# Kernel tuning notes

Hardware: AMD Instinct MI355X
Metric: run time of the kernel (lower is better)

## Reference

```python
import jax, jax.numpy as jnp
import numpy as np

DIM = 1024          # dim_feature
NUM_CLUSTERS = 8
N_PER = 4096        # patches per cluster (equal-size clusters)
NUM_SAMPLE = 1024   # num_sample_feature
QDIM = 128          # q projection dim
# sample_ratio = NUM_SAMPLE / (NUM_CLUSTERS*N_PER) = 1/32 -> top_k per cluster
TOPK = int(np.rint(N_PER * NUM_SAMPLE / (NUM_CLUSTERS * N_PER)))  # 128


def setup_inputs() -> dict:
    key = jax.random.key(0)
    ks = jax.random.split(key, 6)
    s = 1.0 / np.sqrt(DIM)
    return {
        "cluster_features": jax.random.normal(ks[0], (NUM_CLUSTERS, N_PER, DIM), jnp.float32),
        "key_feats": jax.random.normal(ks[1], (NUM_CLUSTERS, 1, DIM), jnp.float32),
        "q_w": jax.random.normal(ks[2], (QDIM, DIM), jnp.float32) * s,
        "q_b": jax.random.normal(ks[3], (QDIM,), jnp.float32) * 0.01,
        "v_w": jax.random.normal(ks[4], (DIM, DIM), jnp.float32) * s,
        "v_b": jax.random.normal(ks[5], (DIM,), jnp.float32) * 0.01,
    }


def reference(cluster_features, key_feats, q_w, q_b, v_w, v_b):
    scale_q = jnp.sqrt(jnp.float32(QDIM))

    def per_cluster(feats, key_feat):
        # NonLocalRanking with top_k=TOPK, top_fuse=False (adaptive path)
        Q = feats @ q_w.T + q_b            # [N, 128]
        qk = key_feat @ q_w.T + q_b        # [1, 128]
        A = (Q @ qk.T) / scale_q           # [N, 1]
        A = jax.nn.softmax(A, axis=0)      # softmax over patches (dim 0)
        _, idx = jax.lax.top_k(A[:, 0], TOPK)
        top_feats = feats[idx]             # [TOPK, DIM]
        V = feats @ v_w.T + v_b            # [N, DIM]
        fusion = (A.T @ V)[0]              # [DIM]
        return top_feats, fusion

    tops, fus = jax.vmap(per_cluster)(cluster_features, key_feats)
    selected = tops.reshape(-1, DIM)       # [NUM_CLUSTERS*TOPK, DIM] == [NUM_SAMPLE, DIM]
    # module pads/truncates to NUM_SAMPLE; here it is exactly NUM_SAMPLE
    selected = selected[:NUM_SAMPLE]
    return selected, fus
```

## Files before the change

### kernel.cpp

```cpp
#include <hip/hip_runtime.h>
#include <math.h>


#define DIM   1024
#define NC    8
#define NPER  4096
#define QD    128
#define TOPK  128
#define K1B   128

typedef unsigned long long u64;
typedef __attribute__((ext_vector_type(2))) unsigned long long ull2;
typedef __attribute__((ext_vector_type(4))) float f4;

__global__ __launch_bounds__(256) void k0_prep(
    const float* __restrict__ key_feats, const float* __restrict__ q_w,
    const float* __restrict__ q_b, float* __restrict__ w_all)
{
    const int c  = blockIdx.x >> 2, jc = blockIdx.x & 3;
    const int tid = threadIdx.x;
    __shared__ float part[256];
    __shared__ float qs[QD];

    {
        const int k = tid >> 1, half = tid & 1;
        const float4* qr4 = (const float4*)(q_w + (size_t)k * DIM + half * 512);
        const float4* kf4 = (const float4*)(key_feats + (size_t)c * DIM + half * 512);
        float s = 0.f;
        #pragma unroll 16
        for (int j = 0; j < 128; ++j) {
            float4 a = qr4[j], b = kf4[j];
            s += a.x*b.x + a.y*b.y + a.z*b.z + a.w*b.w;
        }
        part[tid] = s;
    }
    __syncthreads();
    if (tid < QD) qs[tid] = part[2*tid] + part[2*tid+1] + q_b[tid];
    __syncthreads();

    const int j = jc * 256 + tid;
    float s = 0.f;
    #pragma unroll 16
    for (int k = 0; k < QD; ++k)
        s += q_w[(size_t)k * DIM + j] * qs[k];
    w_all[c * DIM + j] = s * 0.08838834764831845f;
}

__global__ __launch_bounds__(256, 4) void k1_main(
    const float* __restrict__ feats, const float* __restrict__ w_all,
    u64* __restrict__ keys,
    float* __restrict__ pacc,
    float* __restrict__ pm, float* __restrict__ pz)
{
    const int c    = blockIdx.y;
    const int blk  = blockIdx.x;
    const int tid  = threadIdx.x;
    const int lane = tid & 63;
    const int wave = tid >> 6;

    const float4* w4 = (const float4*)(w_all + c * DIM);
    float4 wv[4];
    #pragma unroll
    for (int q = 0; q < 4; ++q) wv[q] = w4[lane + 64*q];

    float4 acc[4];
    #pragma unroll
    for (int q = 0; q < 4; ++q) acc[q] = make_float4(0.f, 0.f, 0.f, 0.f);
    float m = -INFINITY, Z = 0.f;

    const int wslot = blk * 4 + wave;
    const float* fc = feats + (size_t)c * NPER * DIM;

    f4 fA[4], fB[4];
    {
        const f4* f4p = (const f4*)(fc + (size_t)wslot * DIM);
        #pragma unroll
        for (int q = 0; q < 4; ++q) fA[q] = __builtin_nontemporal_load(f4p + lane + 64*q);
    }

    #define K1_PROCESS(FREG, ROW)                                              \
    do {                                                                       \
        float p = 0.f;                                                         \
        _Pragma("unroll")                                                      \
        for (int q = 0; q < 4; ++q)                                            \
            p += FREG[q].x*wv[q].x + FREG[q].y*wv[q].y +                       \
                 FREG[q].z*wv[q].z + FREG[q].w*wv[q].w;                        \
        _Pragma("unroll")                                                      \
        for (int off = 32; off > 0; off >>= 1) p += __shfl_xor(p, off, 64);    \
        if (lane == 0) {                                                       \
            unsigned int b = __float_as_uint(p);                               \
            unsigned int u = b ^ ((b & 0x80000000u) ? 0xFFFFFFFFu : 0x80000000u); \
            keys[c * NPER + (ROW)] = ((u64)u << 32) | (unsigned int)(~(ROW));  \
        }                                                                      \
        if (p > m) {                  \
            const float sOld = __expf(m - p);                                  \
            Z = Z * sOld + 1.f;                                                \
            _Pragma("unroll")                                                  \
            for (int q = 0; q < 4; ++q) {                                      \
                acc[q].x = acc[q].x * sOld + FREG[q].x;                        \
                acc[q].y = acc[q].y * sOld + FREG[q].y;                        \
                acc[q].z = acc[q].z * sOld + FREG[q].z;                        \
                acc[q].w = acc[q].w * sOld + FREG[q].w;                        \
            }                                                                  \
            m = p;                                                             \
        } else {                                                               \
            const float t = __expf(p - m);                                     \
            Z += t;                                                            \
            _Pragma("unroll")                                                  \
            for (int q = 0; q < 4; ++q) {                                      \
                acc[q].x += t * FREG[q].x;                                     \
                acc[q].y += t * FREG[q].y;                                     \
                acc[q].z += t * FREG[q].z;                                     \
                acc[q].w += t * FREG[q].w;                                     \
            }                                                                  \
        }                                                                      \
    } while (0)

    for (int it = 0; it < 8; it += 2) {
        const int r0 = wslot + 512 * it;
        {
            const f4* f4p = (const f4*)(fc + (size_t)(r0 + 512) * DIM);
            #pragma unroll
            for (int q = 0; q < 4; ++q) fB[q] = __builtin_nontemporal_load(f4p + lane + 64*q);
        }
        K1_PROCESS(fA, r0);
        if (it + 2 < 8) {
            const f4* f4p = (const f4*)(fc + (size_t)(r0 + 1024) * DIM);
            #pragma unroll
            for (int q = 0; q < 4; ++q) fA[q] = __builtin_nontemporal_load(f4p + lane + 64*q);
        }
        K1_PROCESS(fB, r0 + 512);
    }
    #undef K1_PROCESS

    __shared__ float sm[4], sz[4];
    __shared__ float sacc[4][DIM];
    if (lane == 0) { sm[wave] = m; sz[wave] = Z; }
    #pragma unroll
    for (int q = 0; q < 4; ++q)
        ((float4*)sacc[wave])[lane + 64*q] = acc[q];
    __syncthreads();

    const float mb = fmaxf(fmaxf(sm[0], sm[1]), fmaxf(sm[2], sm[3]));
    const float e0 = __expf(sm[0] - mb), e1 = __expf(sm[1] - mb);
    const float e2 = __expf(sm[2] - mb), e3 = __expf(sm[3] - mb);
    float4 a0 = ((float4*)sacc[0])[tid];
    float4 a1 = ((float4*)sacc[1])[tid];
    float4 a2 = ((float4*)sacc[2])[tid];
    float4 a3 = ((float4*)sacc[3])[tid];
    float4 o;
    o.x = a0.x*e0 + a1.x*e1 + a2.x*e2 + a3.x*e3;
    o.y = a0.y*e0 + a1.y*e1 + a2.y*e2 + a3.y*e3;
    o.z = a0.z*e0 + a1.z*e1 + a2.z*e2 + a3.z*e3;
    o.w = a0.w*e0 + a1.w*e1 + a2.w*e2 + a3.w*e3;
    ((float4*)(pacc + (size_t)(c * K1B + blk) * DIM))[tid] = o;
    if (tid == 0) {
        pm[c * K1B + blk] = mb;
        pz[c * K1B + blk] = sz[0]*e0 + sz[1]*e1 + sz[2]*e2 + sz[3]*e3;
    }
}

__global__ __launch_bounds__(256) void fat_a(
    const float* __restrict__ pacc, const float* __restrict__ pm,
    const float* __restrict__ pz, float* __restrict__ g,
    const u64* __restrict__ keys, int* __restrict__ selIdx)
{
    const int tid = threadIdx.x;
    if (blockIdx.x < 32) {
        const int c = blockIdx.x >> 2, jb = blockIdx.x & 3;
        const int slot = tid & 63;
        const int bg   = tid >> 6;
        __shared__ float spm[K1B], spz[K1B], swe[K1B];
        __shared__ float szc;
        __shared__ float4 sred[3][64];

        if (tid < K1B) spm[tid] = pm[c*K1B + tid];
        else spz[tid - K1B] = pz[c*K1B + tid - K1B];
        __syncthreads();
        float mc = -INFINITY;
        for (int b = 0; b < K1B; ++b) mc = fmaxf(mc, spm[b]);
        if (tid < K1B) swe[tid] = __expf(spm[tid] - mc);
        __syncthreads();
        if (tid == 0) {
            float z = 0.f;
            for (int b = 0; b < K1B; ++b) z += spz[b] * swe[b];
            szc = z;
        }

        const int jbase = jb * 256 + slot * 4;
        float4 a = make_float4(0.f, 0.f, 0.f, 0.f);
        #pragma unroll
        for (int k = 0; k < 32; ++k) {
            const int b = bg * 32 + k;
            const float e = swe[b];
            float4 v = *(const float4*)(pacc + (size_t)(c*K1B + b) * DIM + jbase);
            a.x += e*v.x; a.y += e*v.y; a.z += e*v.z; a.w += e*v.w;
        }
        if (bg) sred[bg-1][slot] = a;
        __syncthreads();
        if (bg == 0) {
            float4 t0 = sred[0][slot], t1 = sred[1][slot], t2 = sred[2][slot];
            const float inv = 1.0f / szc;
            float4 o;
            o.x = (a.x + t0.x + t1.x + t2.x) * inv;
            o.y = (a.y + t0.y + t1.y + t2.y) * inv;
            o.z = (a.z + t0.z + t1.z + t2.z) * inv;
            o.w = (a.w + t0.w + t1.w + t2.w) * inv;
            *(float4*)(g + c * DIM + jbase) = o;
        }
    } else {
        const int c = blockIdx.x - 32;
        __shared__ u64 lk[NPER];
        __shared__ int hist[4096];
        __shared__ unsigned short cand[NPER];
        __shared__ int chunkSuf[256];
        __shared__ int critBin, candCnt;

        for (int t = tid; t < NPER/2; t += 256)
            ((ull2*)lk)[t] = ((const ull2*)(keys + (size_t)c * NPER))[t];
        for (int t = tid; t < 4096; t += 256) hist[t] = 0;
        if (tid == 0) candCnt = 0;
        __syncthreads();

        #pragma unroll
        for (int q = 0; q < 16; ++q)
            atomicAdd(&hist[(int)(lk[tid + 256*q] >> 52)], 1);
        __syncthreads();

        {
            int s = 0;
            #pragma unroll
            for (int b = 0; b < 16; ++b) s += hist[tid*16 + b];
            chunkSuf[tid] = s;
        }
        __syncthreads();
        if (tid == 0) {
            int run = 0;
            for (int t = 255; t >= 0; --t) {
                const int v = chunkSuf[t]; chunkSuf[t] = run; run += v;
            }
        }
        __syncthreads();
        {
            int run = chunkSuf[tid];
            for (int b = 15; b >= 0; --b) {
                const int bin = tid*16 + b;
                const int h = hist[bin];
                if (run < TOPK && run + h >= TOPK) critBin = bin;
                run += h;
            }
        }
        __syncthreads();
        const int B = critBin;

        #pragma unroll
        for (int q = 0; q < 16; ++q) {
            const int i = tid + 256*q;
            if ((int)(lk[i] >> 52) >= B) {
                const int s = atomicAdd(&candCnt, 1);
                cand[s] = (unsigned short)i;
            }
        }
        __syncthreads();

        const int M = candCnt;
        for (int s = tid; s < M; s += 256) {
            const int i = (int)cand[s];
            const u64 ki = lk[i];
            int r = 0;
            for (int j = 0; j < M; ++j)
                r += (lk[(int)cand[j]] > ki) ? 1 : 0;
            if (r < TOPK) selIdx[c * TOPK + r] = i;
        }
    }
}

__global__ __launch_bounds__(256) void fat_b(
    const int* __restrict__ selIdx, const float* __restrict__ feats,
    float* __restrict__ out_sel,
    const float* __restrict__ v_w, const float* __restrict__ v_b,
    const float* __restrict__ g, float* __restrict__ fus)
{
    const int tid = threadIdx.x;
    if (blockIdx.x < 128) {
        const int c  = blockIdx.x >> 4;
        const int r0 = (blockIdx.x & 15) * 8;
        const float* fc = feats + (size_t)c * NPER * DIM;
        const int* sic = selIdx + c * TOPK + r0;

        f4 cur = __builtin_nontemporal_load(
            (const f4*)(fc + (size_t)sic[0] * DIM) + tid);
        #pragma unroll
        for (int s = 0; s < 8; ++s) {
            f4 nxt;
            if (s + 1 < 8)
                nxt = __builtin_nontemporal_load(
                    (const f4*)(fc + (size_t)sic[s+1] * DIM) + tid);
            __builtin_nontemporal_store(
                cur, (f4*)(out_sel + ((size_t)c * TOPK + r0 + s) * DIM) + tid);
            if (s + 1 < 8) cur = nxt;
        }
    } else {
        __shared__ float4 sg[NC][256];
        const int lane = tid & 63, wave = tid >> 6;
        for (int t = tid; t < NC * 256; t += 256)
            ((float4*)sg)[t] = ((const float4*)g)[t];
        __syncthreads();

        const int row0 = (blockIdx.x - 128) * 8 + wave * 2;
        for (int rr = 0; rr < 2; ++rr) {
            const int o = row0 + rr;
            const float4* vr = (const float4*)(v_w + (size_t)o * DIM);
            float4 v[4];
            #pragma unroll
            for (int u = 0; u < 4; ++u) v[u] = vr[lane + 64*u];
            float p[NC];
            #pragma unroll
            for (int cc = 0; cc < NC; ++cc) {
                float s = 0.f;
                #pragma unroll
                for (int u = 0; u < 4; ++u) {
                    float4 gv = sg[cc][lane + 64*u];
                    s += v[u].x*gv.x + v[u].y*gv.y + v[u].z*gv.z + v[u].w*gv.w;
                }
                p[cc] = s;
            }
            #pragma unroll
            for (int off = 32; off > 0; off >>= 1) {
                #pragma unroll
                for (int cc = 0; cc < NC; ++cc) p[cc] += __shfl_xor(p[cc], off, 64);
            }
            if (lane == 0) {
                const float b = v_b[o];
                #pragma unroll
                for (int cc = 0; cc < NC; ++cc) fus[cc * DIM + o] = p[cc] + b;
            }
        }
    }
}

extern "C" void kernel_launch(void* const* d_in, const int* in_sizes, int n_in,
                              void* d_out, int out_size, void* d_ws, size_t ws_size,
                              hipStream_t stream) {
    const float* feats     = (const float*)d_in[0];
    const float* key_feats = (const float*)d_in[1];
    const float* q_w       = (const float*)d_in[2];
    const float* q_b       = (const float*)d_in[3];
    const float* v_w       = (const float*)d_in[4];
    const float* v_b       = (const float*)d_in[5];
    float* out      = (float*)d_out;
    float* out_sel  = out;
    float* out_fus  = out + (size_t)1024 * 1024;

    u64*   keys   = (u64*)d_ws;
    float* pacc   = (float*)(keys + NC * NPER);
    float* pm     = pacc + (size_t)NC * K1B * DIM;
    float* pz     = pm + NC * K1B;
    float* g      = pz + NC * K1B;
    float* w_all  = g + NC * DIM;
    int*   selIdx = (int*)(w_all + NC * DIM);

    k0_prep <<<dim3(NC * 4),  256, 0, stream>>>(key_feats, q_w, q_b, w_all);
    k1_main <<<dim3(K1B, NC), 256, 0, stream>>>(feats, w_all, keys, pacc, pm, pz);
    fat_a   <<<dim3(32 + NC), 256, 0, stream>>>(pacc, pm, pz, g, keys, selIdx);
    fat_b   <<<dim3(256),     256, 0, stream>>>(selIdx, feats, out_sel, v_w, v_b, g, out_fus);
}
```

Baseline: 235.7 us.

## Fuse reduce/top-k and gather/projection kernels via cooperative grid sync

Merges the two tail kernels into one cooperative kernel with a grid-wide barrier, removing a launch boundary. The fusion reduction is spread across 128 blocks instead of 32, and blocks that are idle in phase one prefetch their v_w rows into registers before the barrier. The cost is cooperative launch overhead, a grid sync, and a larger shared-memory union that may limit co-residency.

```diff
diff --git a/kernel.cpp b/kernel.cpp
--- a/kernel.cpp
+++ b/kernel.cpp
@@ -1,5 +1,8 @@
 #include <hip/hip_runtime.h>
+#include <hip/hip_cooperative_groups.h>
 #include <math.h>
+
+namespace cg = cooperative_groups;
 
 
 #define DIM   1024
@@ -160,22 +163,39 @@
     }
 }
 
-__global__ __launch_bounds__(256) void fat_a(
+__global__ __launch_bounds__(256) void fat_ab(
     const float* __restrict__ pacc, const float* __restrict__ pm,
     const float* __restrict__ pz, float* __restrict__ g,
-    const u64* __restrict__ keys, int* __restrict__ selIdx)
+    const u64* __restrict__ keys, int* __restrict__ selIdx,
+    const float* __restrict__ feats, float* __restrict__ out_sel,
+    const float* __restrict__ v_w, const float* __restrict__ v_b,
+    float* __restrict__ fus)
 {
+    const int bid = blockIdx.x;
     const int tid = threadIdx.x;
-    if (blockIdx.x < 32) {
-        const int c = blockIdx.x >> 2, jb = blockIdx.x & 3;
-        const int slot = tid & 63;
-        const int bg   = tid >> 6;
-        __shared__ float spm[K1B], spz[K1B], swe[K1B];
-        __shared__ float szc;
-        __shared__ float4 sred[3][64];
-
-        if (tid < K1B) spm[tid] = pm[c*K1B + tid];
-        else spz[tid - K1B] = pz[c*K1B + tid - K1B];
+    __shared__ float4 shraw4[3649];
+
+    float4 vpre0[4], vpre1[4];
+    const bool kpre = (bid >= 136);
+    if (kpre) {
+        const int lane = tid & 63, wave = tid >> 6;
+        const int row0 = (bid - 128) * 8 + wave * 2;
+        const float4* vr0 = (const float4*)(v_w + (size_t)row0 * DIM);
+        const float4* vr1 = (const float4*)(v_w + (size_t)(row0 + 1) * DIM);
+        #pragma unroll
+        for (int u = 0; u < 4; ++u) { vpre0[u] = vr0[lane + 64*u]; vpre1[u] = vr1[lane + 64*u]; }
+    }
+
+    if (bid < 128) {
+        const int c = bid >> 4, jb = bid & 15;
+        float* spm = (float*)shraw4;
+        float* spz = spm + 128;
+        float* swe = spz + 128;
+        float* szc = swe + 128;
+        float4* sred = (float4*)(szc + 4);
+
+        if (tid < K1B)       spm[tid]       = pm[c*K1B + tid];
+        else                 spz[tid - K1B] = pz[c*K1B + tid - K1B];
         __syncthreads();
         float mc = -INFINITY;
         for (int b = 0; b < K1B; ++b) mc = fmaxf(mc, spm[b]);
@@ -184,42 +204,45 @@
         if (tid == 0) {
             float z = 0.f;
             for (int b = 0; b < K1B; ++b) z += spz[b] * swe[b];
-            szc = z;
-        }
-
-        const int jbase = jb * 256 + slot * 4;
+            *szc = z;
+        }
+        const int col = tid & 15;
+        const int bg  = tid >> 4;
+        const int jbase = jb * 64 + col * 4;
         float4 a = make_float4(0.f, 0.f, 0.f, 0.f);
         #pragma unroll
-        for (int k = 0; k < 32; ++k) {
-            const int b = bg * 32 + k;
+        for (int k = 0; k < 8; ++k) {
+            const int b = bg * 8 + k;
             const float e = swe[b];
             float4 v = *(const float4*)(pacc + (size_t)(c*K1B + b) * DIM + jbase);
             a.x += e*v.x; a.y += e*v.y; a.z += e*v.z; a.w += e*v.w;
         }
-        if (bg) sred[bg-1][slot] = a;
-        __syncthreads();
-        if (bg == 0) {
-            float4 t0 = sred[0][slot], t1 = sred[1][slot], t2 = sred[2][slot];
-            const float inv = 1.0f / szc;
-            float4 o;
-            o.x = (a.x + t0.x + t1.x + t2.x) * inv;
-            o.y = (a.y + t0.y + t1.y + t2.y) * inv;
-            o.z = (a.z + t0.z + t1.z + t2.z) * inv;
-            o.w = (a.w + t0.w + t1.w + t2.w) * inv;
-            *(float4*)(g + c * DIM + jbase) = o;
-        }
-    } else {
-        const int c = blockIdx.x - 32;
-        __shared__ u64 lk[NPER];
-        __shared__ int hist[4096];
-        __shared__ unsigned short cand[NPER];
-        __shared__ int chunkSuf[256];
-        __shared__ int critBin, candCnt;
+        sred[bg * 16 + col] = a;
+        __syncthreads();
+        if (tid < 16) {
+            float4 o = make_float4(0.f, 0.f, 0.f, 0.f);
+            #pragma unroll
+            for (int gg = 0; gg < 16; ++gg) {
+                float4 t = sred[gg * 16 + tid];
+                o.x += t.x; o.y += t.y; o.z += t.z; o.w += t.w;
+            }
+            const float inv = 1.0f / (*szc);
+            o.x *= inv; o.y *= inv; o.z *= inv; o.w *= inv;
+            *(float4*)(g + c * DIM + jb * 64 + tid * 4) = o;
+        }
+    } else if (bid < 136) {
+        const int c = bid - 128;
+        u64* lk = (u64*)shraw4;
+        int* hist = (int*)(lk + NPER);
+        unsigned short* cand = (unsigned short*)(hist + 4096);
+        int* chunkSuf = (int*)(cand + NPER);
+        int* critBin = chunkSuf + 256;
+        int* candCnt = critBin + 1;
 
         for (int t = tid; t < NPER/2; t += 256)
             ((ull2*)lk)[t] = ((const ull2*)(keys + (size_t)c * NPER))[t];
         for (int t = tid; t < 4096; t += 256) hist[t] = 0;
-        if (tid == 0) candCnt = 0;
+        if (tid == 0) *candCnt = 0;
         __syncthreads();
 
         #pragma unroll
@@ -246,24 +269,24 @@
             for (int b = 15; b >= 0; --b) {
                 const int bin = tid*16 + b;
                 const int h = hist[bin];
-                if (run < TOPK && run + h >= TOPK) critBin = bin;
+                if (run < TOPK && run + h >= TOPK) *critBin = bin;
                 run += h;
             }
         }
         __syncthreads();
-        const int B = critBin;
+        const int B = *critBin;
 
         #pragma unroll
         for (int q = 0; q < 16; ++q) {
             const int i = tid + 256*q;
             if ((int)(lk[i] >> 52) >= B) {
-                const int s = atomicAdd(&candCnt, 1);
+                const int s = atomicAdd(candCnt, 1);
                 cand[s] = (unsigned short)i;
             }
         }
         __syncthreads();
 
-        const int M = candCnt;
+        const int M = *candCnt;
         for (int s = tid; s < M; s += 256) {
             const int i = (int)cand[s];
             const u64 ki = lk[i];
@@ -273,18 +296,13 @@
             if (r < TOPK) selIdx[c * TOPK + r] = i;
         }
     }
-}
-
-__global__ __launch_bounds__(256) void fat_b(
-    const int* __restrict__ selIdx, const float* __restrict__ feats,
-    float* __restrict__ out_sel,
-    const float* __restrict__ v_w, const float* __restrict__ v_b,
-    const float* __restrict__ g, float* __restrict__ fus)
-{
-    const int tid = threadIdx.x;
-    if (blockIdx.x < 128) {
-        const int c  = blockIdx.x >> 4;
-        const int r0 = (blockIdx.x & 15) * 8;
+
+    __threadfence();
+    cg::this_grid().sync();
+
+    if (bid < 128) {
+        const int c  = bid >> 4;
+        const int r0 = (bid & 15) * 8;
         const float* fc = feats + (size_t)c * NPER * DIM;
         const int* sic = selIdx + c * TOPK + r0;
 
@@ -301,26 +319,33 @@
             if (s + 1 < 8) cur = nxt;
         }
     } else {
-        __shared__ float4 sg[NC][256];
+        float4* sg = shraw4;
         const int lane = tid & 63, wave = tid >> 6;
+        __syncthreads();
         for (int t = tid; t < NC * 256; t += 256)
-            ((float4*)sg)[t] = ((const float4*)g)[t];
-        __syncthreads();
-
-        const int row0 = (blockIdx.x - 128) * 8 + wave * 2;
+            sg[t] = ((const float4*)g)[t];
+        __syncthreads();
+
+        const int row0 = (bid - 128) * 8 + wave * 2;
+        #pragma unroll
         for (int rr = 0; rr < 2; ++rr) {
             const int o = row0 + rr;
-            const float4* vr = (const float4*)(v_w + (size_t)o * DIM);
             float4 v[4];
-            #pragma unroll
-            for (int u = 0; u < 4; ++u) v[u] = vr[lane + 64*u];
+            if (kpre) {
+                #pragma unroll
+                for (int u = 0; u < 4; ++u) v[u] = rr ? vpre1[u] : vpre0[u];
+            } else {
+                const float4* vr = (const float4*)(v_w + (size_t)o * DIM);
+                #pragma unroll
+                for (int u = 0; u < 4; ++u) v[u] = vr[lane + 64*u];
+            }
             float p[NC];
             #pragma unroll
             for (int cc = 0; cc < NC; ++cc) {
                 float s = 0.f;
                 #pragma unroll
                 for (int u = 0; u < 4; ++u) {
-                    float4 gv = sg[cc][lane + 64*u];
+                    float4 gv = sg[cc * 256 + lane + 64*u];
                     s += v[u].x*gv.x + v[u].y*gv.y + v[u].z*gv.z + v[u].w*gv.w;
                 }
                 p[cc] = s;
@@ -362,6 +387,9 @@
 
     k0_prep <<<dim3(NC * 4),  256, 0, stream>>>(key_feats, q_w, q_b, w_all);
     k1_main <<<dim3(K1B, NC), 256, 0, stream>>>(feats, w_all, keys, pacc, pm, pz);
-    fat_a   <<<dim3(32 + NC), 256, 0, stream>>>(pacc, pm, pz, g, keys, selIdx);
-    fat_b   <<<dim3(256),     256, 0, stream>>>(selIdx, feats, out_sel, v_w, v_b, g, out_fus);
+
+    void* args[] = { (void*)&pacc, (void*)&pm, (void*)&pz, (void*)&g,
+                     (void*)&keys, (void*)&selIdx, (void*)&feats,
+                     (void*)&out_sel, (void*)&v_w, (void*)&v_b, (void*)&out_fus };
+    hipLaunchCooperativeKernel(fat_ab, dim3(256), dim3(256), args, 0, stream);
 }
```

Measured after the change: 306.8 us. 30.2% more time.
